# Kernel optimization log

Measured on AMD Instinct MI355X. Metric: run time of the kernel, lower is better.

## Reference

```python
import jax, jax.numpy as jnp
import numpy as np

N_HEADS = 16

def setup_inputs() -> dict:
    key = jax.random.key(0)
    k1, k2, k3 = jax.random.split(key, 3)
    B, T, C = 4, 2048, 1024
    x = jax.random.normal(k1, (B, T, C), dtype=jnp.float32)
    w_qkv = jax.random.normal(k2, (C, 3 * C), dtype=jnp.float32) * (1.0 / np.sqrt(C))
    w_out = jax.random.normal(k3, (C, C), dtype=jnp.float32) * (1.0 / np.sqrt(C))
    return {"x": x, "w_qkv": w_qkv, "w_out": w_out}

def reference(x, w_qkv, w_out):
    B, T, C = x.shape
    H = N_HEADS
    D = C // H
    qkv = jnp.einsum('btc,cf->btf', x, w_qkv).reshape(B, T, 3, H, D)
    q, k, v = qkv[:, :, 0], qkv[:, :, 1], qkv[:, :, 2]  # [B,T,H,D]
    q = q.transpose(0, 2, 1, 3)  # [B,H,T,D]
    k = k.transpose(0, 2, 1, 3)
    v = v.transpose(0, 2, 1, 3)
    scale = 1.0 / jnp.sqrt(jnp.asarray(D, dtype=x.dtype))
    scores = jnp.einsum('bhqd,bhkd->bhqk', q, k) * scale  # [B,H,T,T]
    causal = jnp.tril(jnp.ones((T, T), dtype=bool))
    scores = jnp.where(causal[None, None], scores, jnp.asarray(-jnp.inf, dtype=scores.dtype))
    attn = jax.nn.softmax(scores, axis=-1)
    ctx = jnp.einsum('bhqk,bhkd->bhqd', attn, v)  # [B,H,T,D]
    ctx = ctx.transpose(0, 2, 1, 3).reshape(B, T, C)
    return jnp.einsum('btc,co->bto', ctx, w_out)
```

## Files before the change

### kernel.cpp

```cpp
#include <hip/hip_runtime.h>

typedef __attribute__((ext_vector_type(8))) short bf16x8;
typedef __attribute__((ext_vector_type(4))) short bf16x4;
typedef __attribute__((ext_vector_type(4))) float f32x4;
typedef __attribute__((ext_vector_type(4))) unsigned short u16x4;

#define MFMA16(a, b, c) __builtin_amdgcn_mfma_f32_16x16x32_bf16((a), (b), (c), 0, 0, 0)
#define MFMA16K16(a, b, c) __builtin_amdgcn_mfma_f32_16x16x16bf16_1k((a), (b), (c), 0, 0, 0)

__device__ __forceinline__ unsigned short f2bf(float f) {
    union { float f; unsigned int u; } x; x.f = f;
    unsigned int r = x.u + 0x7FFFu + ((x.u >> 16) & 1u);
    return (unsigned short)(r >> 16);
}
__device__ __forceinline__ unsigned int fbits(float f) {
    union { float f; unsigned int u; } x; x.f = f;
    return x.u;
}
__device__ __forceinline__ void gload_lds16(const void* g, void* l) {
    __builtin_amdgcn_global_load_lds(
        (const __attribute__((address_space(1))) unsigned int*)g,
        (__attribute__((address_space(3))) unsigned int*)l,
        16, 0, 0);
}

__global__ void cast_x(const float* __restrict__ in, unsigned short* __restrict__ hi,
                       int n) {
    int i = (blockIdx.x * blockDim.x + threadIdx.x) * 4;
    if (i >= n) return;
    float4 v = *(const float4*)(in + i);
    float vv[4] = {v.x, v.y, v.z, v.w};
    u16x4 h;
#pragma unroll
    for (int j = 0; j < 4; ++j) h[j] = f2bf(vv[j]);
    *(u16x4*)(hi + i) = h;
}

__global__ void tcast_k(const float* __restrict__ in, unsigned short* __restrict__ out,
                        int K, int N) {
    __shared__ float tile[64][65];
    int n0 = blockIdx.x * 64, k0 = blockIdx.y * 64;
    for (int i = threadIdx.x; i < 4096; i += 256) {
        int r = i >> 6, c = i & 63;
        tile[r][c] = in[(size_t)(k0 + r) * N + n0 + c];
    }
    __syncthreads();
    for (int i = threadIdx.x; i < 4096; i += 256) {
        int r = i >> 6, c = i & 63;
        out[(size_t)(n0 + r) * K + k0 + c] = f2bf(tile[c][r]);
    }
}

__global__ __launch_bounds__(256, 2) void gemm_qkv(
    const unsigned short* __restrict__ A,
    const unsigned short* __restrict__ Bt,
    unsigned short* __restrict__ qout, unsigned short* __restrict__ kout,
    unsigned short* __restrict__ vtout) {
    const int K = 1024;
    __shared__ __align__(16) unsigned short sA[128 * 64], sB[128 * 64];
    int tid = threadIdx.x, lane = tid & 63, w = tid >> 6;
    int c = lane & 15, quad = lane >> 4;
    int sw = c & 7;
    int wm = (w >> 1) * 64, wn = (w & 1) * 64;
    int m0 = blockIdx.y * 128, n0 = blockIdx.x * 128;

    f32x4 acc[4][4];
#pragma unroll
    for (int i = 0; i < 4; i++)
#pragma unroll
        for (int j = 0; j < 4; j++) acc[i][j] = (f32x4){0.f, 0.f, 0.f, 0.f};

    for (int kk = 0; kk < K; kk += 64) {
#pragma unroll
        for (int p = 0; p < 4; ++p) {
            int ch = p * 256 + tid;
            int r = ch >> 3;
            int gs = (ch & 7) ^ (r & 7);
            gload_lds16(A + (size_t)(m0 + r) * K + kk + gs * 8, &sA[ch * 8]);
            gload_lds16(Bt + (size_t)(n0 + r) * K + kk + gs * 8, &sB[ch * 8]);
        }
        __syncthreads();
#pragma unroll
        for (int ks8 = 0; ks8 < 8; ks8 += 4) {
            bf16x8 af[4], bfr[4];
#pragma unroll
            for (int mt = 0; mt < 4; ++mt)
                af[mt] = *(const bf16x8*)&sA[(wm + mt * 16 + c) * 64 +
                                             ((ks8 + quad) ^ sw) * 8];
#pragma unroll
            for (int nt = 0; nt < 4; ++nt)
                bfr[nt] = *(const bf16x8*)&sB[(wn + nt * 16 + c) * 64 +
                                              ((ks8 + quad) ^ sw) * 8];
#pragma unroll
            for (int mt = 0; mt < 4; ++mt)
#pragma unroll
                for (int nt = 0; nt < 4; ++nt)
                    acc[mt][nt] = MFMA16(af[mt], bfr[nt], acc[mt][nt]);
        }
        __syncthreads();
    }

    const float QSCALE = 0.1803368801111601f;
#pragma unroll
    for (int mt = 0; mt < 4; ++mt) {
#pragma unroll
        for (int nt = 0; nt < 4; ++nt) {
#pragma unroll
            for (int r = 0; r < 4; ++r) {
                int row = m0 + wm + mt * 16 + quad * 4 + r;
                int col = n0 + wn + nt * 16 + c;
                float v = acc[mt][nt][r];
                int which = col >> 10;
                int h = (col >> 6) & 15;
                int d = col & 63;
                int b = row >> 11;
                int t = row & 2047;
                size_t bh_ = (size_t)(b * 16 + h);
                if (which == 0)
                    qout[(bh_ * 2048 + t) * 64 + d] = f2bf(v * QSCALE);
                else if (which == 1)
                    kout[(bh_ * 2048 + t) * 64 + d] = f2bf(v);
                else
                    vtout[(bh_ * 64 + d) * 2048 + t] = f2bf(v);
            }
        }
    }
}

__global__ __launch_bounds__(256, 2) void gemm2_bt(
    const unsigned short* __restrict__ A,
    const unsigned short* __restrict__ Bt,
    float* __restrict__ out) {
    const int K = 1024, N = 1024;
    __shared__ __align__(16) unsigned short sA[128 * 64], sB[128 * 64];
    int tid = threadIdx.x, lane = tid & 63, w = tid >> 6;
    int c = lane & 15, quad = lane >> 4;
    int sw = c & 7;
    int wm = (w >> 1) * 64, wn = (w & 1) * 64;
    int m0 = blockIdx.y * 128, n0 = blockIdx.x * 128;

    f32x4 acc[4][4];
#pragma unroll
    for (int i = 0; i < 4; i++)
#pragma unroll
        for (int j = 0; j < 4; j++) acc[i][j] = (f32x4){0.f, 0.f, 0.f, 0.f};

    for (int kk = 0; kk < K; kk += 64) {
#pragma unroll
        for (int p = 0; p < 4; ++p) {
            int ch = p * 256 + tid;
            int r = ch >> 3;
            int gs = (ch & 7) ^ (r & 7);
            gload_lds16(A + (size_t)(m0 + r) * K + kk + gs * 8, &sA[ch * 8]);
            gload_lds16(Bt + (size_t)(n0 + r) * K + kk + gs * 8, &sB[ch * 8]);
        }
        __syncthreads();
#pragma unroll
        for (int ks8 = 0; ks8 < 8; ks8 += 4) {
            bf16x8 af[4], bfr[4];
#pragma unroll
            for (int mt = 0; mt < 4; ++mt)
                af[mt] = *(const bf16x8*)&sA[(wm + mt * 16 + c) * 64 +
                                             ((ks8 + quad) ^ sw) * 8];
#pragma unroll
            for (int nt = 0; nt < 4; ++nt)
                bfr[nt] = *(const bf16x8*)&sB[(wn + nt * 16 + c) * 64 +
                                              ((ks8 + quad) ^ sw) * 8];
#pragma unroll
            for (int mt = 0; mt < 4; ++mt)
#pragma unroll
                for (int nt = 0; nt < 4; ++nt)
                    acc[mt][nt] = MFMA16(af[mt], bfr[nt], acc[mt][nt]);
        }
        __syncthreads();
    }

#pragma unroll
    for (int mt = 0; mt < 4; ++mt)
#pragma unroll
        for (int nt = 0; nt < 4; ++nt)
#pragma unroll
            for (int r = 0; r < 4; ++r) {
                int row = m0 + wm + mt * 16 + quad * 4 + r;
                int col = n0 + wn + nt * 16 + c;
                out[(size_t)row * N + col] = acc[mt][nt][r];
            }
}

#define SSTR 72
__device__ const int JOB_ORDER[24] = {7, 15, 23, 14, 22, 6,  13, 21, 12, 20, 5,  11,
                                      19, 10, 18, 4,  9,  17, 8,  16, 3,  2,  1,  0};

__global__ __launch_bounds__(256, 4) void attn_k(
    const unsigned short* __restrict__ q,
    const unsigned short* __restrict__ k,
    const unsigned short* __restrict__ vt,
    unsigned short* __restrict__ ctx,
    float* __restrict__ op, float* __restrict__ lbuf) {
    const int T = 2048, D = 64;
    __shared__ __align__(16) unsigned short sK[2][64 * SSTR];
    __shared__ __align__(16) unsigned short sV[2][64 * SSTR];

    int tid = threadIdx.x, lane = tid & 63, w = tid >> 6;
    int c = lane & 15, quad = lane >> 4;

    int rank = blockIdx.x >> 6, bh = blockIdx.x & 63;
    int t = JOB_ORDER[rank];
    int jt, kt0, nkt;
    bool split, has_diag;
    if (t < 8)        { jt = t;     kt0 = 0;      nkt = 2 * t + 2; split = false; has_diag = true; }
    else if (t < 16)  { jt = t;     kt0 = 0;      nkt = jt + 1;    split = true;  has_diag = false; }
    else              { jt = t - 8; kt0 = jt + 1; nkt = jt + 1;    split = true;  has_diag = true; }
    int kt_end = kt0 + nkt;
    int b = bh >> 4, hh = bh & 15;

    const unsigned short* qh = q + (size_t)bh * T * D;
    const unsigned short* kh = k + (size_t)bh * T * D;
    const unsigned short* vh = vt + (size_t)bh * D * T;

    int dv = tid >> 3, tcv = (tid & 7) * 8;
    int q0 = jt * 128;
    int qloc = w * 16 + c;
    int qrow[2];
    qrow[0] = q0 + qloc;
    qrow[1] = qrow[0] + 64;

    bf16x8 bq[2][2];
#pragma unroll
    for (int g = 0; g < 2; ++g) {
        bq[g][0] = *(const bf16x8*)&qh[(size_t)qrow[g] * D + quad * 8];
        bq[g][1] = *(const bf16x8*)&qh[(size_t)qrow[g] * D + 32 + quad * 8];
    }

    f32x4 o[2][4];
#pragma unroll
    for (int g = 0; g < 2; ++g)
#pragma unroll
        for (int nt = 0; nt < 4; ++nt) o[g][nt] = (f32x4){0.f, 0.f, 0.f, 0.f};
    float l_i[2] = {0.f, 0.f};

    int kb0 = kt0 * 64;
    bf16x8 kr0 = *(const bf16x8*)&kh[(size_t)(kb0 + lane) * D + w * 8];
    bf16x8 kr1 = *(const bf16x8*)&kh[(size_t)(kb0 + lane) * D + w * 8 + 32];
    bf16x8 vr0 = *(const bf16x8*)&vh[(size_t)dv * T + kb0 + tcv];
    bf16x8 vr1 = *(const bf16x8*)&vh[(size_t)(dv + 32) * T + kb0 + tcv];
    *(bf16x8*)&sK[0][lane * SSTR + w * 8] = kr0;
    *(bf16x8*)&sK[0][lane * SSTR + w * 8 + 32] = kr1;
    *(bf16x8*)&sV[0][dv * SSTR + tcv] = vr0;
    *(bf16x8*)&sV[0][(dv + 32) * SSTR + tcv] = vr1;
    __syncthreads();

    int cur = 0;
    for (int kt = kt0; kt < kt_end; ++kt) {
        int kb = kt * 64;
        if (kt + 1 < kt_end) {
            int kb2 = kb + 64;
            kr0 = *(const bf16x8*)&kh[(size_t)(kb2 + lane) * D + w * 8];
            kr1 = *(const bf16x8*)&kh[(size_t)(kb2 + lane) * D + w * 8 + 32];
            vr0 = *(const bf16x8*)&vh[(size_t)dv * T + kb2 + tcv];
            vr1 = *(const bf16x8*)&vh[(size_t)(dv + 32) * T + kb2 + tcv];
        }
        bool g0_active = !has_diag || (kt != 2 * jt + 1);

        const unsigned short* sKc = sK[cur];
        const unsigned short* sVc = sV[cur];

        f32x4 st[2][4];
        __builtin_amdgcn_s_setprio(1);
#pragma unroll
        for (int mt = 0; mt < 4; ++mt) {
            bf16x8 ak0 = *(const bf16x8*)&sKc[(mt * 16 + c) * SSTR + quad * 8];
            bf16x8 ak1 = *(const bf16x8*)&sKc[(mt * 16 + c) * SSTR + 32 + quad * 8];
#pragma unroll
            for (int g = 0; g < 2; ++g) {
                f32x4 z = (f32x4){0.f, 0.f, 0.f, 0.f};
                z = MFMA16(ak0, bq[g][0], z);
                z = MFMA16(ak1, bq[g][1], z);
                st[g][mt] = z;
            }
        }
        __builtin_amdgcn_s_setprio(0);

        bf16x4 pf[2][4];
#pragma unroll
        for (int g = 0; g < 2; ++g) {
            if (g == 0 && !g0_active) continue;
            bool diag = has_diag && (kb == q0 + (g << 6));
            if (diag) {
#pragma unroll
                for (int mt = 0; mt < 4; ++mt)
#pragma unroll
                    for (int r = 0; r < 4; ++r)
                        if (mt * 16 + quad * 4 + r > qloc) st[g][mt][r] = -1.0e30f;
            }
            float rs = 0.f;
#pragma unroll
            for (int mt = 0; mt < 4; ++mt) {
                float p0 = __builtin_exp2f(st[g][mt][0]);
                float p1 = __builtin_exp2f(st[g][mt][1]);
                float p2 = __builtin_exp2f(st[g][mt][2]);
                float p3 = __builtin_exp2f(st[g][mt][3]);
                rs += (p0 + p1) + (p2 + p3);
                unsigned int w0 = __builtin_amdgcn_perm(
                    fbits(p1) + 0x8000u, fbits(p0) + 0x8000u, 0x07060302u);
                unsigned int w1 = __builtin_amdgcn_perm(
                    fbits(p3) + 0x8000u, fbits(p2) + 0x8000u, 0x07060302u);
                uint2 pk; pk.x = w0; pk.y = w1;
                pf[g][mt] = *(bf16x4*)&pk;
            }
            l_i[g] += rs;
        }

        __builtin_amdgcn_s_setprio(1);
#pragma unroll
        for (int mt = 0; mt < 4; ++mt) {
#pragma unroll
            for (int nt = 0; nt < 4; ++nt) {
                bf16x4 av = *(const bf16x4*)&sVc[(nt * 16 + c) * SSTR + mt * 16 + quad * 4];
                if (g0_active) o[0][nt] = MFMA16K16(av, pf[0][mt], o[0][nt]);
                o[1][nt] = MFMA16K16(av, pf[1][mt], o[1][nt]);
            }
        }
        __builtin_amdgcn_s_setprio(0);

        if (kt + 1 < kt_end) {
            int nxt = cur ^ 1;
            *(bf16x8*)&sK[nxt][lane * SSTR + w * 8] = kr0;
            *(bf16x8*)&sK[nxt][lane * SSTR + w * 8 + 32] = kr1;
            *(bf16x8*)&sV[nxt][dv * SSTR + tcv] = vr0;
            *(bf16x8*)&sV[nxt][(dv + 32) * SSTR + tcv] = vr1;
            __syncthreads();
            cur = nxt;
        }
    }

    if (!split) {
#pragma unroll
        for (int g = 0; g < 2; ++g) {
            float l = l_i[g];
            l += __shfl_xor(l, 16);
            l += __shfl_xor(l, 32);
            float inv = 1.0f / l;
#pragma unroll
            for (int nt = 0; nt < 4; ++nt) {
                u16x4 ob;
#pragma unroll
                for (int r = 0; r < 4; ++r) ob[r] = f2bf(o[g][nt][r] * inv);
                *(u16x4*)&ctx[(size_t)(b * T + qrow[g]) * 1024 + hh * 64 + nt * 16 + quad * 4] = ob;
            }
        }
    } else {
        int piece = has_diag ? 1 : 0;
        int sidx = bh * 8 + (jt - 8);
        size_t base = (size_t)(piece * 512 + sidx) * 128;
#pragma unroll
        for (int g = 0; g < 2; ++g) {
            float l = l_i[g];
            l += __shfl_xor(l, 16);
            l += __shfl_xor(l, 32);
            int rloc = qrow[g] - q0;
            if (quad == 0) lbuf[base + rloc] = l;
            float* orow = op + (base + rloc) * 64;
#pragma unroll
            for (int nt = 0; nt < 4; ++nt)
                *(f32x4*)&orow[nt * 16 + quad * 4] = o[g][nt];
        }
    }
}

__global__ void merge_k(const float* __restrict__ op, const float* __restrict__ lbuf,
                        unsigned short* __restrict__ ctx) {
    int gid = blockIdx.x * 256 + threadIdx.x;
    int row = gid >> 4, dq = (gid & 15) * 4;
    int sidx = row >> 7, rloc = row & 127;
    int bh = sidx >> 3, jt = 8 + (sidx & 7);
    int b = bh >> 4, hh = bh & 15;
    int tq = jt * 128 + rloc;
    float inv = 1.0f / (lbuf[row] + lbuf[65536 + row]);
    float4 o0 = *(const float4*)(op + (size_t)row * 64 + dq);
    float4 o1 = *(const float4*)(op + (size_t)(65536 + row) * 64 + dq);
    u16x4 ob;
    ob[0] = f2bf((o0.x + o1.x) * inv);
    ob[1] = f2bf((o0.y + o1.y) * inv);
    ob[2] = f2bf((o0.z + o1.z) * inv);
    ob[3] = f2bf((o0.w + o1.w) * inv);
    *(u16x4*)&ctx[((size_t)(b * 2048 + tq)) * 1024 + hh * 64 + dq] = ob;
}

extern "C" void kernel_launch(void* const* d_in, const int* in_sizes, int n_in,
                              void* d_out, int out_size, void* d_ws, size_t ws_size,
                              hipStream_t stream) {
    const float* x     = (const float*)d_in[0];
    const float* w_qkv = (const float*)d_in[1];
    const float* w_out = (const float*)d_in[2];
    float* out = (float*)d_out;

    char* ws = (char*)d_ws;
    unsigned short* wqkvt = (unsigned short*)(ws + 0);
    unsigned short* woutt = (unsigned short*)(ws + 6291456);
    unsigned short* x_bf  = (unsigned short*)(ws + 8388608);
    unsigned short* qb    = (unsigned short*)(ws + 25165824);
    unsigned short* kb    = (unsigned short*)(ws + 41943040);
    unsigned short* vtb   = (unsigned short*)(ws + 58720256);
    unsigned short* ctx   = (unsigned short*)(ws + 8388608);

    float* op   = (float*)d_out;
    float* lbuf = (float*)ws;

    cast_x<<<8192, 256, 0, stream>>>(x, x_bf, 8388608);
    tcast_k<<<dim3(48, 16), 256, 0, stream>>>(w_qkv, wqkvt, 1024, 3072);
    tcast_k<<<dim3(16, 16), 256, 0, stream>>>(w_out, woutt, 1024, 1024);
    gemm_qkv<<<dim3(24, 64), 256, 0, stream>>>(x_bf, wqkvt, qb, kb, vtb);
    attn_k<<<1536, 256, 0, stream>>>(qb, kb, vtb, ctx, op, lbuf);
    merge_k<<<4096, 256, 0, stream>>>(op, lbuf, ctx);
    gemm2_bt<<<dim3(8, 64), 256, 0, stream>>>(ctx, woutt, out);
}
```

Before: 269.5 us.

## Stage QKV epilogue through LDS for vectorized stores and remap blocks across XCDs

The QKV GEMM epilogue now writes bf16 results into a padded shared-memory tile, transposed for the V slice, and then emits 16-byte vector stores to the q, k and transposed-v outputs. Previously each lane stored scattered 2-byte values, which was especially costly for the strided V transpose. Both GEMMs also remap the workgroup index so that consecutive tiles land on the same XCD, aiming for better L2 reuse of A and B tiles. The change adds an extra barrier and reuses the operand LDS buffers, enlarged to 17408 shorts, for the epilogue tile.

New measurement: 264.6 us. No clear change (-1.8%).

```diff
diff --git a/kernel.cpp b/kernel.cpp
--- a/kernel.cpp
+++ b/kernel.cpp
@@ -57,12 +57,18 @@
     unsigned short* __restrict__ qout, unsigned short* __restrict__ kout,
     unsigned short* __restrict__ vtout) {
     const int K = 1024;
-    __shared__ __align__(16) unsigned short sA[128 * 64], sB[128 * 64];
+    __shared__ __align__(16) unsigned short smem[17408];
+    unsigned short* sA = smem;
+    unsigned short* sB = smem + 8192;
     int tid = threadIdx.x, lane = tid & 63, w = tid >> 6;
     int c = lane & 15, quad = lane >> 4;
     int sw = c & 7;
     int wm = (w >> 1) * 64, wn = (w & 1) * 64;
-    int m0 = blockIdx.y * 128, n0 = blockIdx.x * 128;
+
+    int wg = blockIdx.y * 24 + blockIdx.x;
+    int nid = (wg & 7) * 192 + (wg >> 3);
+    int m_blk = nid / 24, n_blk = nid - m_blk * 24;
+    int m0 = m_blk * 128, n0 = n_blk * 128;
 
     f32x4 acc[4][4];
 #pragma unroll
@@ -101,28 +107,55 @@
     }
 
     const float QSCALE = 0.1803368801111601f;
-#pragma unroll
-    for (int mt = 0; mt < 4; ++mt) {
-#pragma unroll
-        for (int nt = 0; nt < 4; ++nt) {
-#pragma unroll
-            for (int r = 0; r < 4; ++r) {
-                int row = m0 + wm + mt * 16 + quad * 4 + r;
-                int col = n0 + wn + nt * 16 + c;
-                float v = acc[mt][nt][r];
-                int which = col >> 10;
-                int h = (col >> 6) & 15;
-                int d = col & 63;
-                int b = row >> 11;
-                int t = row & 2047;
-                size_t bh_ = (size_t)(b * 16 + h);
-                if (which == 0)
-                    qout[(bh_ * 2048 + t) * 64 + d] = f2bf(v * QSCALE);
-                else if (which == 1)
-                    kout[(bh_ * 2048 + t) * 64 + d] = f2bf(v);
-                else
-                    vtout[(bh_ * 64 + d) * 2048 + t] = f2bf(v);
-            }
+    bool vreg = (n0 >= 2048);
+    if (!vreg) {
+        float scale = (n0 < 1024) ? QSCALE : 1.0f;
+#pragma unroll
+        for (int mt = 0; mt < 4; ++mt)
+#pragma unroll
+            for (int nt = 0; nt < 4; ++nt)
+#pragma unroll
+                for (int r = 0; r < 4; ++r)
+                    smem[(wm + mt * 16 + quad * 4 + r) * 136 + wn + nt * 16 + c] =
+                        f2bf(acc[mt][nt][r] * scale);
+    } else {
+#pragma unroll
+        for (int mt = 0; mt < 4; ++mt)
+#pragma unroll
+            for (int nt = 0; nt < 4; ++nt)
+#pragma unroll
+                for (int r = 0; r < 4; ++r)
+                    smem[(wn + nt * 16 + c) * 136 + wm + mt * 16 + quad * 4 + r] =
+                        f2bf(acc[mt][nt][r]);
+    }
+    __syncthreads();
+
+    int rr = tid >> 4, cc = tid & 15;
+    if (!vreg) {
+        int col = n0 + cc * 8;
+        int which = col >> 10;
+        int h = (col >> 6) & 15, d = col & 63;
+        unsigned short* dst = which ? kout : qout;
+#pragma unroll
+        for (int j = 0; j < 8; ++j) {
+            int row = rr + j * 16;
+            int grow = m0 + row;
+            int b = grow >> 11, t = grow & 2047;
+            size_t bh_ = (size_t)(b * 16 + h);
+            bf16x8 vv = *(const bf16x8*)&smem[row * 136 + cc * 8];
+            *(bf16x8*)&dst[(bh_ * 2048 + t) * 64 + d] = vv;
+        }
+    } else {
+        int grow = m0 + cc * 8;
+        int b = grow >> 11, t = grow & 2047;
+#pragma unroll
+        for (int j = 0; j < 8; ++j) {
+            int nrow = rr + j * 16;
+            int col = n0 + nrow;
+            int h = (col >> 6) & 15, d = col & 63;
+            size_t bh_ = (size_t)(b * 16 + h);
+            bf16x8 vv = *(const bf16x8*)&smem[nrow * 136 + cc * 8];
+            *(bf16x8*)&vtout[(bh_ * 64 + d) * 2048 + t] = vv;
         }
     }
 }
@@ -137,7 +170,11 @@
     int c = lane & 15, quad = lane >> 4;
     int sw = c & 7;
     int wm = (w >> 1) * 64, wn = (w & 1) * 64;
-    int m0 = blockIdx.y * 128, n0 = blockIdx.x * 128;
+
+    int wg = blockIdx.y * 8 + blockIdx.x;
+    int nid = (wg & 7) * 64 + (wg >> 3);
+    int m_blk = nid >> 3, n_blk = nid & 7;
+    int m0 = m_blk * 128, n0 = n_blk * 128;
 
     f32x4 acc[4][4];
 #pragma unroll
```
